# Performance work log

Measured on AMD Instinct MI355X. Metric: run time of the kernel, lower is better.

## Reference

```python
import jax, jax.numpy as jnp
import numpy as np

# Real spherical harmonics for l=0,1,2 in 'component' normalization (sqrt(4*pi) * Y_std),
# m ordered -l..l per l, matching the e3nn Kernel's norm_Y = sqrt(4*pi)*I convention.
_SQ3 = 3.0 ** 0.5
_SQ5 = 5.0 ** 0.5
_SQ15 = 15.0 ** 0.5

def sph_harm_012(d):
    # d: [N,3] unit directions -> Y: [N,9]
    x, y, z = d[:, 0], d[:, 1], d[:, 2]
    one = jnp.ones_like(x)
    return jnp.stack([
        one,                      # l=0
        _SQ3 * y,                 # l=1, m=-1
        _SQ3 * z,                 # l=1, m=0
        _SQ3 * x,                 # l=1, m=1
        _SQ15 * x * y,            # l=2, m=-2
        _SQ15 * y * z,            # l=2, m=-1
        0.5 * _SQ5 * (3.0 * z * z - 1.0),  # l=2, m=0
        _SQ15 * x * z,            # l=2, m=1
        0.5 * _SQ15 * (x * x - y * y),     # l=2, m=2
    ], axis=1)


def setup_inputs() -> dict:
    key = jax.random.key(0)
    ks = jax.random.split(key, 7)
    N, I, J, Y, W, H = 65536, 16, 16, 9, 96, 128
    return {
        "r": jax.random.normal(ks[0], (N, 3), dtype=jnp.float32),
        "Q": jax.random.normal(ks[1], (I, J, Y, W), dtype=jnp.float32) * 0.1,
        "W1": jax.random.normal(ks[2], (1, H), dtype=jnp.float32),
        "b1": jax.random.normal(ks[3], (H,), dtype=jnp.float32),
        "W2": jax.random.normal(ks[4], (H, W), dtype=jnp.float32) * (1.0 / H ** 0.5),
        "b2": jax.random.normal(ks[5], (W,), dtype=jnp.float32),
        "K0": jax.random.normal(ks[6], (I, J), dtype=jnp.float32),
    }


def reference(r, Q, W1, b1, W2, b2, K0):
    R_EPS = 0.0
    radii = jnp.linalg.norm(r, axis=1)              # [N]
    mask = radii > R_EPS                            # [N]
    safe = jnp.where(mask, radii, 1.0)
    d = r / safe[:, None]                           # unit directions [N,3]
    Ysh = sph_harm_012(d)                           # [N,9]
    # Radial MLP: R -> R^w
    h = jax.nn.relu(radii[:, None] * W1[0][None, :] + b1)  # [N,H]
    Rad = h @ W2 + b2                               # [N,96]
    # kernel1 = einsum('ijyw,zy,zw->zij', Q, Y, R)
    k1 = jnp.einsum('ijyw,zy,zw->zij', Q, Ysh, Rad, optimize=True)  # [N,16,16]
    # scatter-by-mask: points at/below r_eps get the self-interaction kernel K0
    return jnp.where(mask[:, None, None], k1, K0[None, :, :])
```

## Files before the change

kernel.cpp:

```cpp
#include <hip/hip_runtime.h>
#include <hip/hip_bf16.h>


typedef __attribute__((ext_vector_type(8)))  short bfrag;
typedef __attribute__((ext_vector_type(16))) float fx16;

#define WS_TB  0
#define WS_ABT 512
#define WS_QP  50048

__device__ inline unsigned short f2bf(float f) {
  union { float f; unsigned int u; } v; v.f = f;
  unsigned int r = v.u + 0x7FFFu + ((v.u >> 16) & 1u);
  return (unsigned short)(r >> 16);
}
__device__ inline unsigned int pack2(float a, float b) {
  return (unsigned int)f2bf(a) | ((unsigned int)f2bf(b) << 16);
}
__device__ inline float bf_lo(unsigned int v) {
  union { unsigned int u; float f; } c; c.u = v << 16; return c.f;
}
__device__ inline float bf_hi(unsigned int v) {
  union { unsigned int u; float f; } c; c.u = v & 0xFFFF0000u; return c.f;
}
__device__ inline unsigned int cvtpk(float a, float b) {
  unsigned int d;
  asm("v_cvt_pk_bf16_f32 %0, %1, %2" : "=v"(d) : "v"(a), "v"(b));
  return d;
}

__device__ inline void gl_lds16(const void* g, void* l) {
  __builtin_amdgcn_global_load_lds(
      (const __attribute__((address_space(1))) unsigned int*)g,
      (__attribute__((address_space(3))) unsigned int*)l, 16, 0, 0);
}

__global__ void k_prep(const float* __restrict__ Q,
                       const float* __restrict__ W1, const float* __restrict__ b1,
                       const float* __restrict__ W2, const float* __restrict__ b2,
                       float* __restrict__ tb, unsigned int* __restrict__ ABt,
                       unsigned short* __restrict__ qp) {
  const int tid = threadIdx.x;
  if (blockIdx.x != 0) {
    int u = (blockIdx.x - 1) * 256 + tid;
    int c128 = u & 127;
    int hl   = (u >> 7) & 1;
    int ks   = (u >> 8) & 1;
    int cbf  = (u >> 9) & 1;
    int kcp  = u >> 10;
    int wbi  = kcp / 9, y = kcp - wbi * 9;
    int c    = cbf * 128 + c128;
    int k    = y * 96 + wbi * 32 + ks * 16 + hl * 8;
    const float4* s = (const float4*)(Q + c * 864 + k);
    float4 a = s[0], b = s[1];
    uint4 o;
    o.x = pack2(a.x, a.y); o.y = pack2(a.z, a.w);
    o.z = pack2(b.x, b.y); o.w = pack2(b.z, b.w);
    *(uint4*)(qp + (size_t)u * 8) = o;
    return;
  }
  __shared__ float w2_s[128 * 96];
  __shared__ float val_s[128], stb_s[128], w1_s[128], b1_s[128];
  __shared__ int   perm_s[128];
  for (int i = tid; i < 128 * 96; i += 256) w2_s[i] = W2[i];
  const float INF = __builtin_inff();
  if (tid < 128) {
    float w1 = W1[tid], b1v = b1[tid];
    w1_s[tid] = w1; b1_s[tid] = b1v;
    float tj = -b1v / w1;
    bool valid = (w1 != 0.0f) && (tj > 0.0f);
    val_s[tid] = valid ? tj : INF;
  }
  __syncthreads();
  if (tid < 128) {
    float v = val_s[tid];
    int rank = 0;
    for (int m = 0; m < 128; ++m) {
      float vm = val_s[m];
      rank += (vm < v || (vm == v && m < tid)) ? 1 : 0;
    }
    stb_s[rank] = v; perm_s[rank] = tid;
  }
  __syncthreads();
  if (tid < 128) tb[tid] = stb_s[tid];
  if (tid < 96) {
    float s0  = stb_s[0];
    float tm0 = (s0 == INF) ? 1.0f : 0.5f * s0;
    float sa = 0.f, sb = 0.f;
#pragma unroll 8
    for (int j = 0; j < 128; ++j) {
      float on = (tm0 * w1_s[j] + b1_s[j] > 0.0f) ? 1.f : 0.f;
      float w2 = on * w2_s[j * 96 + tid];
      sa += w2 * w1_s[j]; sb += w2 * b1_s[j];
    }
    float b2v = b2[tid];
    ABt[tid] = pack2(sa, sb + b2v);
#pragma unroll 8
    for (int s = 0; s < 128; ++s) {
      int   j    = perm_s[s];
      float live = (stb_s[s] < INF) ? 1.f : 0.f;
      float sgn  = (w1_s[j] > 0.f) ? live : -live;
      float w2   = sgn * w2_s[j * 96 + tid];
      sa += w2 * w1_s[j]; sb += w2 * b1_s[j];
      ABt[(s + 1) * 96 + tid] = pack2(sa, sb + b2v);
    }
  }
}

#define RSTR 104

__global__ __launch_bounds__(256, 2)
void k_main(const float* __restrict__ r, const float* __restrict__ tbg,
            const unsigned int* __restrict__ ABt,
            const unsigned short* __restrict__ qp, const float* __restrict__ K0,
            float* __restrict__ out) {
  __shared__ unsigned short Rad_s[256][RSTR];
  __shared__ float Ysh_s[256][9];
  __shared__ unsigned short Bb[2][4096];
  __shared__ float tb_s[128];
  __shared__ float radii_s[256];

  const int tid  = threadIdx.x;
  const int lane = tid & 63;
  const int wave = tid >> 6;
  const int hl   = lane >> 5;
  const int l31  = lane & 31;
  const int zb   = blockIdx.x >> 1;
  const int cb   = blockIdx.x & 1;
  const int z0   = zb * 256;
  const char* qg = (const char*)qp;

  {
    const char* g = qg + (size_t)cb * 8192 + wave * 2048 + lane * 16;
    char* l = ((char*)&Bb[0][0]) + wave * 2048;
    gl_lds16(g, l);
    gl_lds16(g + 1024, l + 1024);
  }
  if (tid < 128) tb_s[tid] = tbg[tid];

  const int row = tid, z = z0 + row;
  {
    float rx = r[z * 3 + 0], ry = r[z * 3 + 1], rz = r[z * 3 + 2];
    float rad = sqrtf(rx * rx + ry * ry + rz * rz);
    radii_s[row] = rad;
    float inv = (rad > 0.f) ? (1.0f / rad) : 1.0f;
    float x = rx * inv, y = ry * inv, zc = rz * inv;
    const float SQ3 = 1.7320508075688772f, SQ5 = 2.2360679774997896f,
                SQ15 = 3.872983346207417f;
    Ysh_s[row][0] = 1.f;
    Ysh_s[row][1] = SQ3 * y;
    Ysh_s[row][2] = SQ3 * zc;
    Ysh_s[row][3] = SQ3 * x;
    Ysh_s[row][4] = SQ15 * x * y;
    Ysh_s[row][5] = SQ15 * y * zc;
    Ysh_s[row][6] = 0.5f * SQ5 * (3.f * zc * zc - 1.f);
    Ysh_s[row][7] = SQ15 * x * zc;
    Ysh_s[row][8] = 0.5f * SQ15 * (x * x - y * y);
    __syncthreads();
    int lo = 0, hi = 128;
    while (lo < hi) { int mid = (lo + hi) >> 1;
                      if (tb_s[mid] < rad) lo = mid + 1; else hi = mid; }
    const uint4* abv = (const uint4*)(ABt + lo * 96);
#pragma unroll
    for (int gq = 0; gq < 12; ++gq) {
      uint4 u0 = abv[2 * gq], u1 = abv[2 * gq + 1];
      float r0 = fmaf(bf_lo(u0.x), rad, bf_hi(u0.x));
      float r1 = fmaf(bf_lo(u0.y), rad, bf_hi(u0.y));
      float r2 = fmaf(bf_lo(u0.z), rad, bf_hi(u0.z));
      float r3 = fmaf(bf_lo(u0.w), rad, bf_hi(u0.w));
      float r4 = fmaf(bf_lo(u1.x), rad, bf_hi(u1.x));
      float r5 = fmaf(bf_lo(u1.y), rad, bf_hi(u1.y));
      float r6 = fmaf(bf_lo(u1.z), rad, bf_hi(u1.z));
      float r7 = fmaf(bf_lo(u1.w), rad, bf_hi(u1.w));
      uint4 o;
      o.x = pack2(r0, r1); o.y = pack2(r2, r3);
      o.z = pack2(r4, r5); o.w = pack2(r6, r7);
      *(uint4*)(&Rad_s[row][gq * 8]) = o;
    }
  }
  __syncthreads();

  const int row0 = wave * 64 + l31;
  const int row1 = row0 + 32;

  float ys0[9], ys1[9];
#pragma unroll
  for (int j = 0; j < 9; ++j) { ys0[j] = Ysh_s[row0][j]; ys1[j] = Ysh_s[row1][j]; }

  fx16 acc[2][4];
#pragma unroll
  for (int ri = 0; ri < 2; ++ri)
#pragma unroll
    for (int j = 0; j < 4; ++j)
#pragma unroll
      for (int e = 0; e < 16; ++e) acc[ri][j][e] = 0.f;

  const int bfo = hl * 2048 + l31 * 16;

  for (int wbi = 0; wbi < 3; ++wbi) {
    const int wb = wbi * 32;
    const uint4 w00 = *(const uint4*)(&Rad_s[row0][wb + hl * 8]);
    const uint4 w01 = *(const uint4*)(&Rad_s[row0][wb + 16 + hl * 8]);
    const uint4 w10 = *(const uint4*)(&Rad_s[row1][wb + hl * 8]);
    const uint4 w11 = *(const uint4*)(&Rad_s[row1][wb + 16 + hl * 8]);
#pragma unroll
    for (int y = 0; y < 9; ++y) {
      const int p = wbi * 9 + y;
      if (p + 1 < 27) {
        const char* g = qg + (size_t)((p + 1) * 2 + cb) * 8192 + wave * 2048 + lane * 16;
        char* l = ((char*)&Bb[(p + 1) & 1][0]) + wave * 2048;
        gl_lds16(g, l);
        gl_lds16(g + 1024, l + 1024);
      }
      const unsigned short* bbuf = &Bb[p & 1][0];
      const float Y0 = ys0[y], Y1 = ys1[y];
#pragma unroll
      for (int ks = 0; ks < 2; ++ks) {
        const uint4 u0 = ks ? w01 : w00;
        const uint4 u1 = ks ? w11 : w10;
        uint4 p0, p1;
        p0.x = cvtpk(bf_lo(u0.x) * Y0, bf_hi(u0.x) * Y0);
        p0.y = cvtpk(bf_lo(u0.y) * Y0, bf_hi(u0.y) * Y0);
        p0.z = cvtpk(bf_lo(u0.z) * Y0, bf_hi(u0.z) * Y0);
        p0.w = cvtpk(bf_lo(u0.w) * Y0, bf_hi(u0.w) * Y0);
        p1.x = cvtpk(bf_lo(u1.x) * Y1, bf_hi(u1.x) * Y1);
        p1.y = cvtpk(bf_lo(u1.y) * Y1, bf_hi(u1.y) * Y1);
        p1.z = cvtpk(bf_lo(u1.z) * Y1, bf_hi(u1.z) * Y1);
        p1.w = cvtpk(bf_lo(u1.w) * Y1, bf_hi(u1.w) * Y1);
        union { uint4 u; bfrag f; } ua, ub;
        ua.u = p0; ub.u = p1;
        const bfrag a0 = ua.f, a1 = ub.f;
        const char* bp = (const char*)bbuf + ks * 4096 + bfo;
#pragma unroll
        for (int j = 0; j < 4; ++j) {
          union { uint4 u; bfrag f; } bj;
          bj.u = *(const uint4*)(bp + j * 512);
          acc[0][j] = __builtin_amdgcn_mfma_f32_32x32x16_bf16(a0, bj.f, acc[0][j], 0, 0, 0);
          acc[1][j] = __builtin_amdgcn_mfma_f32_32x32x16_bf16(a1, bj.f, acc[1][j], 0, 0, 0);
        }
      }
      __syncthreads();
    }
  }

  float k0v[4];
#pragma unroll
  for (int j = 0; j < 4; ++j) k0v[j] = K0[cb * 128 + j * 32 + l31];
#pragma unroll
  for (int ri = 0; ri < 2; ++ri) {
#pragma unroll
    for (int rr = 0; rr < 16; ++rr) {
      const int rw = wave * 64 + ri * 32 + (rr & 3) + 8 * (rr >> 2) + 4 * hl;
      const bool m = radii_s[rw] > 0.f;
      const size_t o = (size_t)(z0 + rw) * 256 + cb * 128 + l31;
#pragma unroll
      for (int j = 0; j < 4; ++j)
        out[o + j * 32] = m ? acc[ri][j][rr] : k0v[j];
    }
  }
}

extern "C" void kernel_launch(void* const* d_in, const int* in_sizes, int n_in,
                              void* d_out, int out_size, void* d_ws, size_t ws_size,
                              hipStream_t stream) {
  const float* r  = (const float*)d_in[0];
  const float* Q  = (const float*)d_in[1];
  const float* W1 = (const float*)d_in[2];
  const float* b1 = (const float*)d_in[3];
  const float* W2 = (const float*)d_in[4];
  const float* b2 = (const float*)d_in[5];
  const float* K0 = (const float*)d_in[6];
  float* out = (float*)d_out;
  char* ws = (char*)d_ws;
  float* tb = (float*)(ws + WS_TB);
  unsigned int* ABt = (unsigned int*)(ws + WS_ABT);
  unsigned short* qp = (unsigned short*)(ws + WS_QP);

  hipLaunchKernelGGL(k_prep, dim3(109), dim3(256), 0, stream,
                     Q, W1, b1, W2, b2, tb, ABt, qp);
  hipLaunchKernelGGL(k_main, dim3(512), dim3(256), 0, stream,
                     r, tb, ABt, qp, K0, out);
}
```

Baseline: 61.16 us.

## Use 8 waves per block with one row tile each and triple-buffered Q prefetch

```diff
diff --git a/kernel.cpp b/kernel.cpp
--- a/kernel.cpp
+++ b/kernel.cpp
@@ -28,7 +28,6 @@
   asm("v_cvt_pk_bf16_f32 %0, %1, %2" : "=v"(d) : "v"(a), "v"(b));
   return d;
 }
-
 __device__ inline void gl_lds16(const void* g, void* l) {
   __builtin_amdgcn_global_load_lds(
       (const __attribute__((address_space(1))) unsigned int*)g,
@@ -109,14 +108,13 @@
 
 #define RSTR 104
 
-__global__ __launch_bounds__(256, 2)
+__global__ __launch_bounds__(512, 4)
 void k_main(const float* __restrict__ r, const float* __restrict__ tbg,
             const unsigned int* __restrict__ ABt,
             const unsigned short* __restrict__ qp, const float* __restrict__ K0,
             float* __restrict__ out) {
   __shared__ unsigned short Rad_s[256][RSTR];
-  __shared__ float Ysh_s[256][9];
-  __shared__ unsigned short Bb[2][4096];
+  __shared__ unsigned short Bb[3][4096];
   __shared__ float tb_s[128];
   __shared__ float radii_s[256];
 
@@ -131,38 +129,45 @@
   const char* qg = (const char*)qp;
 
   {
-    const char* g = qg + (size_t)cb * 8192 + wave * 2048 + lane * 16;
-    char* l = ((char*)&Bb[0][0]) + wave * 2048;
-    gl_lds16(g, l);
-    gl_lds16(g + 1024, l + 1024);
+    const char* g0 = qg + (size_t)cb * 8192 + wave * 1024 + lane * 16;
+    gl_lds16(g0, ((char*)&Bb[0][0]) + wave * 1024);
+    const char* g1 = qg + (size_t)(16384 + cb * 8192) + wave * 1024 + lane * 16;
+    gl_lds16(g1, ((char*)&Bb[1][0]) + wave * 1024);
   }
   if (tid < 128) tb_s[tid] = tbg[tid];
 
-  const int row = tid, z = z0 + row;
+  const int myrow = wave * 32 + l31;
+  float ys[9];
   {
-    float rx = r[z * 3 + 0], ry = r[z * 3 + 1], rz = r[z * 3 + 2];
+    const float* rg = r + (size_t)(z0 + myrow) * 3;
+    float rx = rg[0], ry = rg[1], rz = rg[2];
     float rad = sqrtf(rx * rx + ry * ry + rz * rz);
-    radii_s[row] = rad;
     float inv = (rad > 0.f) ? (1.0f / rad) : 1.0f;
     float x = rx * inv, y = ry * inv, zc = rz * inv;
     const float SQ3 = 1.7320508075688772f, SQ5 = 2.2360679774997896f,
                 SQ15 = 3.872983346207417f;
-    Ysh_s[row][0] = 1.f;
-    Ysh_s[row][1] = SQ3 * y;
-    Ysh_s[row][2] = SQ3 * zc;
-    Ysh_s[row][3] = SQ3 * x;
-    Ysh_s[row][4] = SQ15 * x * y;
-    Ysh_s[row][5] = SQ15 * y * zc;
-    Ysh_s[row][6] = 0.5f * SQ5 * (3.f * zc * zc - 1.f);
-    Ysh_s[row][7] = SQ15 * x * zc;
-    Ysh_s[row][8] = 0.5f * SQ15 * (x * x - y * y);
+    ys[0] = 1.f;
+    ys[1] = SQ3 * y;  ys[2] = SQ3 * zc;  ys[3] = SQ3 * x;
+    ys[4] = SQ15 * x * y;  ys[5] = SQ15 * y * zc;
+    ys[6] = 0.5f * SQ5 * (3.f * zc * zc - 1.f);
+    ys[7] = SQ15 * x * zc;
+    ys[8] = 0.5f * SQ15 * (x * x - y * y);
+  }
+
+  {
+    const int prow = tid >> 1, phalf = tid & 1;
+    const float* rg = r + (size_t)(z0 + prow) * 3;
+    float rx = rg[0], ry = rg[1], rz = rg[2];
+    float rad = sqrtf(rx * rx + ry * ry + rz * rz);
+    if (phalf == 0) radii_s[prow] = rad;
     __syncthreads();
     int lo = 0, hi = 128;
     while (lo < hi) { int mid = (lo + hi) >> 1;
                       if (tb_s[mid] < rad) lo = mid + 1; else hi = mid; }
-    const uint4* abv = (const uint4*)(ABt + lo * 96);
-#pragma unroll
-    for (int gq = 0; gq < 12; ++gq) {
+    const uint4* abv = (const uint4*)(ABt + lo * 96 + phalf * 48);
+    const int w0 = phalf * 48;
+#pragma unroll
+    for (int gq = 0; gq < 6; ++gq) {
       uint4 u0 = abv[2 * gq], u1 = abv[2 * gq + 1];
       float r0 = fmaf(bf_lo(u0.x), rad, bf_hi(u0.x));
       float r1 = fmaf(bf_lo(u0.y), rad, bf_hi(u0.y));
@@ -175,88 +180,73 @@
       uint4 o;
       o.x = pack2(r0, r1); o.y = pack2(r2, r3);
       o.z = pack2(r4, r5); o.w = pack2(r6, r7);
-      *(uint4*)(&Rad_s[row][gq * 8]) = o;
-    }
-  }
-  __syncthreads();
-
-  const int row0 = wave * 64 + l31;
-  const int row1 = row0 + 32;
-
-  float ys0[9], ys1[9];
-#pragma unroll
-  for (int j = 0; j < 9; ++j) { ys0[j] = Ysh_s[row0][j]; ys1[j] = Ysh_s[row1][j]; }
-
-  fx16 acc[2][4];
-#pragma unroll
-  for (int ri = 0; ri < 2; ++ri)
+      *(uint4*)(&Rad_s[prow][w0 + gq * 8]) = o;
+    }
+  }
+  asm volatile("s_waitcnt vmcnt(0) lgkmcnt(0)" ::: "memory");
+  __builtin_amdgcn_s_barrier();
+  __builtin_amdgcn_sched_barrier(0);
+
+  fx16 acc[4];
+#pragma unroll
+  for (int j = 0; j < 4; ++j)
+#pragma unroll
+    for (int e = 0; e < 16; ++e) acc[j][e] = 0.f;
+
+  const int bfo = hl * 2048 + l31 * 16;
+  uint4 w00, w01;
+#pragma unroll
+  for (int p = 0; p < 27; ++p) {
+    const int wbi = p / 9, y = p - wbi * 9;
+    if (y == 0) {
+      w00 = *(const uint4*)(&Rad_s[myrow][wbi * 32 + hl * 8]);
+      w01 = *(const uint4*)(&Rad_s[myrow][wbi * 32 + 16 + hl * 8]);
+    }
+    if (p + 2 < 27) {
+      const char* g = qg + (size_t)((p + 2) * 2 + cb) * 8192 + wave * 1024 + lane * 16;
+      gl_lds16(g, ((char*)&Bb[(p + 2) % 3][0]) + wave * 1024);
+    }
+    const float Y0 = ys[y];
+    const char* bbuf = (const char*)&Bb[p % 3][0];
+#pragma unroll
+    for (int ks = 0; ks < 2; ++ks) {
+      const uint4 u0 = ks ? w01 : w00;
+      uint4 pk;
+      pk.x = cvtpk(bf_lo(u0.x) * Y0, bf_hi(u0.x) * Y0);
+      pk.y = cvtpk(bf_lo(u0.y) * Y0, bf_hi(u0.y) * Y0);
+      pk.z = cvtpk(bf_lo(u0.z) * Y0, bf_hi(u0.z) * Y0);
+      pk.w = cvtpk(bf_lo(u0.w) * Y0, bf_hi(u0.w) * Y0);
+      union { uint4 u; bfrag f; } ua; ua.u = pk;
+      const char* bp = bbuf + ks * 4096 + bfo;
+#pragma unroll
+      for (int j = 0; j < 4; ++j) {
+        union { uint4 u; bfrag f; } bj;
+        bj.u = *(const uint4*)(bp + j * 512);
+        acc[j] = __builtin_amdgcn_mfma_f32_32x32x16_bf16(ua.f, bj.f, acc[j], 0, 0, 0);
+      }
+    }
+    if (p + 2 < 27) {
+      asm volatile("s_waitcnt vmcnt(1) lgkmcnt(0)" ::: "memory");
+    } else if (p + 1 < 27) {
+      asm volatile("s_waitcnt vmcnt(0) lgkmcnt(0)" ::: "memory");
+    }
+    if (p + 1 < 27) {
+      __builtin_amdgcn_s_barrier();
+      __builtin_amdgcn_sched_barrier(0);
+    }
+  }
+
+  float k0v[4];
+#pragma unroll
+  for (int j = 0; j < 4; ++j) k0v[j] = K0[cb * 128 + j * 32 + l31];
+#pragma unroll
+  for (int rr = 0; rr < 16; ++rr) {
+    const int rw = wave * 32 + (rr & 3) + 8 * (rr >> 2) + 4 * hl;
+    const bool m = radii_s[rw] > 0.f;
+    const size_t o = (size_t)(z0 + rw) * 256 + cb * 128 + l31;
 #pragma unroll
     for (int j = 0; j < 4; ++j)
-#pragma unroll
-      for (int e = 0; e < 16; ++e) acc[ri][j][e] = 0.f;
-
-  const int bfo = hl * 2048 + l31 * 16;
-
-  for (int wbi = 0; wbi < 3; ++wbi) {
-    const int wb = wbi * 32;
-    const uint4 w00 = *(const uint4*)(&Rad_s[row0][wb + hl * 8]);
-    const uint4 w01 = *(const uint4*)(&Rad_s[row0][wb + 16 + hl * 8]);
-    const uint4 w10 = *(const uint4*)(&Rad_s[row1][wb + hl * 8]);
-    const uint4 w11 = *(const uint4*)(&Rad_s[row1][wb + 16 + hl * 8]);
-#pragma unroll
-    for (int y = 0; y < 9; ++y) {
-      const int p = wbi * 9 + y;
-      if (p + 1 < 27) {
-        const char* g = qg + (size_t)((p + 1) * 2 + cb) * 8192 + wave * 2048 + lane * 16;
-        char* l = ((char*)&Bb[(p + 1) & 1][0]) + wave * 2048;
-        gl_lds16(g, l);
-        gl_lds16(g + 1024, l + 1024);
-      }
-      const unsigned short* bbuf = &Bb[p & 1][0];
-      const float Y0 = ys0[y], Y1 = ys1[y];
-#pragma unroll
-      for (int ks = 0; ks < 2; ++ks) {
-        const uint4 u0 = ks ? w01 : w00;
-        const uint4 u1 = ks ? w11 : w10;
-        uint4 p0, p1;
-        p0.x = cvtpk(bf_lo(u0.x) * Y0, bf_hi(u0.x) * Y0);
-        p0.y = cvtpk(bf_lo(u0.y) * Y0, bf_hi(u0.y) * Y0);
-        p0.z = cvtpk(bf_lo(u0.z) * Y0, bf_hi(u0.z) * Y0);
-        p0.w = cvtpk(bf_lo(u0.w) * Y0, bf_hi(u0.w) * Y0);
-        p1.x = cvtpk(bf_lo(u1.x) * Y1, bf_hi(u1.x) * Y1);
-        p1.y = cvtpk(bf_lo(u1.y) * Y1, bf_hi(u1.y) * Y1);
-        p1.z = cvtpk(bf_lo(u1.z) * Y1, bf_hi(u1.z) * Y1);
-        p1.w = cvtpk(bf_lo(u1.w) * Y1, bf_hi(u1.w) * Y1);
-        union { uint4 u; bfrag f; } ua, ub;
-        ua.u = p0; ub.u = p1;
-        const bfrag a0 = ua.f, a1 = ub.f;
-        const char* bp = (const char*)bbuf + ks * 4096 + bfo;
-#pragma unroll
-        for (int j = 0; j < 4; ++j) {
-          union { uint4 u; bfrag f; } bj;
-          bj.u = *(const uint4*)(bp + j * 512);
-          acc[0][j] = __builtin_amdgcn_mfma_f32_32x32x16_bf16(a0, bj.f, acc[0][j], 0, 0, 0);
-          acc[1][j] = __builtin_amdgcn_mfma_f32_32x32x16_bf16(a1, bj.f, acc[1][j], 0, 0, 0);
-        }
-      }
-      __syncthreads();
-    }
-  }
-
-  float k0v[4];
-#pragma unroll
-  for (int j = 0; j < 4; ++j) k0v[j] = K0[cb * 128 + j * 32 + l31];
-#pragma unroll
-  for (int ri = 0; ri < 2; ++ri) {
-#pragma unroll
-    for (int rr = 0; rr < 16; ++rr) {
-      const int rw = wave * 64 + ri * 32 + (rr & 3) + 8 * (rr >> 2) + 4 * hl;
-      const bool m = radii_s[rw] > 0.f;
-      const size_t o = (size_t)(z0 + rw) * 256 + cb * 128 + l31;
-#pragma unroll
-      for (int j = 0; j < 4; ++j)
-        out[o + j * 32] = m ? acc[ri][j][rr] : k0v[j];
-    }
+      out[o + j * 32] = m ? acc[j][rr] : k0v[j];
   }
 }
 
@@ -278,6 +268,6 @@
 
   hipLaunchKernelGGL(k_prep, dim3(109), dim3(256), 0, stream,
                      Q, W1, b1, W2, b2, tb, ABt, qp);
-  hipLaunchKernelGGL(k_main, dim3(512), dim3(256), 0, stream,
+  hipLaunchKernelGGL(k_main, dim3(512), dim3(512), 0, stream,
                      r, tb, ABt, qp, K0, out);
 }
```

Measured after the change: 57.34 us. -6.3%, faster.
